# Kernel tuning notes

Hardware: AMD Instinct MI355X
Metric: run time of the kernel (lower is better)

## Reference

```python
import jax, jax.numpy as jnp
import numpy as np

TOTAL_MUONS = 2_000_000
BATCH = 16_384
FEAT = 3
COND = 4
NEG = -1.0e9


def _leaky(x):
    return jax.nn.leaky_relu(x, 0.2)


def setup_inputs() -> dict:
    key = jax.random.key(0)
    ks = jax.random.split(key, 12)
    flat_muons = jax.random.normal(ks[0], (TOTAL_MUONS, FEAT), dtype=jnp.float32)
    batch_index = jnp.sort(jax.random.randint(ks[1], (TOTAL_MUONS,), 0, BATCH)).astype(jnp.int64)
    conditions = jax.random.normal(ks[2], (BATCH, COND), dtype=jnp.float32)
    def lin(k, fan_in, fan_out):
        bound = 1.0 / np.sqrt(fan_in)
        kw, kb = jax.random.split(k)
        w = jax.random.uniform(kw, (fan_in, fan_out), jnp.float32, -bound, bound)
        b = jax.random.uniform(kb, (fan_out,), jnp.float32, -bound, bound)
        return w, b
    w1, b1 = lin(ks[3], FEAT + COND, 64)
    w2, b2 = lin(ks[4], 64, 128)
    w3, b3 = lin(ks[5], 128 + COND, 128)
    w4, b4 = lin(ks[6], 128, 1)
    return {"flat_muons": flat_muons, "batch_index": batch_index,
            "conditions": conditions, "batch_size": BATCH,
            "w1": w1, "b1": b1, "w2": w2, "b2": b2,
            "w3": w3, "b3": b3, "w4": w4, "b4": b4}


def reference(flat_muons, batch_index, conditions, batch_size,
              w1, b1, w2, b2, w3, b3, w4, b4):
    # gather event conditions per muon, concat with muon features
    flat_cond = conditions[batch_index]                       # [M, COND]
    point_input = jnp.concatenate([flat_muons, flat_cond], axis=1)
    # point network: Linear -> LeakyReLU(0.2) -> Linear -> LeakyReLU(0.2)
    h = _leaky(point_input @ w1 + b1)
    point_feats = _leaky(h @ w2 + b2)                         # [M, 128]
    point_feats = jnp.nan_to_num(point_feats, nan=0.0, posinf=0.0, neginf=0.0)
    # scatter-reduce amax with init -1e9 (include_self=True semantics)
    seg_max = jax.ops.segment_max(point_feats, batch_index, num_segments=batch_size)
    global_feats = jnp.maximum(seg_max, NEG)                  # [B, 128]
    global_feats = jnp.nan_to_num(global_feats, nan=NEG, posinf=-NEG, neginf=NEG)
    # decision network
    decision_input = jnp.concatenate([global_feats, conditions], axis=1)
    g = _leaky(decision_input @ w3 + b3)
    score = g @ w4 + b4                                       # [B, 1]
    score = score / max(1.0, float(batch_size) ** 0.5)
    return jnp.clip(score, -1000.0, 1000.0)
```

## Files before the change

kernel.cpp:

```cpp
#include <hip/hip_runtime.h>
#include <math.h>

#define NEGF (-1.0e9f)
#define NB 4

typedef __attribute__((ext_vector_type(8))) short short8;
typedef __attribute__((ext_vector_type(4))) float f32x4;

static __device__ __forceinline__ unsigned short bf16_rne(float f) {
    unsigned int u = __float_as_uint(f);
    u += 0x7FFFu + ((u >> 16) & 1u);
    return (unsigned short)(u >> 16);
}

__global__ void seg_bounds_kernel(const int* __restrict__ bi, int M, int B,
                                  int* __restrict__ seg) {
    int m = blockIdx.x * blockDim.x + threadIdx.x;
    if (m >= M) return;
    int cur = bi[m];
    if (m == 0) {
        for (int b = 0; b <= cur; ++b) seg[b] = 0;
    } else {
        int prev = bi[m - 1];
        for (int b = prev + 1; b <= cur; ++b) seg[b] = m;
    }
    if (m == M - 1) {
        for (int b = cur + 1; b <= B; ++b) seg[b] = M;
    }
}

__global__ void prep_w2_kernel(const float* __restrict__ w2,
                               unsigned short* __restrict__ wf) {
    int t = blockIdx.x * blockDim.x + threadIdx.x;
    if (t >= 8192) return;
    int e = t & 7, slot = (t >> 3) & 63, ks = (t >> 9) & 1, cg = t >> 10;
    int lane16 = slot & 15, kg = slot >> 4;
    int k = ks * 32 + kg * 8 + e;
    int col = cg * 16 + lane16;
    float w = w2[k * 128 + col];
    unsigned ub = __float_as_uint(w);
    unsigned short hi = (unsigned short)(ub >> 16);
    float lof = w - __uint_as_float(ub & 0xFFFF0000u);
    unsigned short lo = bf16_rne(lof);
    wf[((cg * 2 + ks) * 2 + 0) * 512 + slot * 8 + e] = hi;
    wf[((cg * 2 + ks) * 2 + 1) * 512 + slot * 8 + e] = lo;
}

__global__ __launch_bounds__(64, 2) void critic_kernel(
    const float* __restrict__ muons,
    const float* __restrict__ conds,
    const int*   __restrict__ seg,
    const float* __restrict__ w1,
    const float* __restrict__ b1,
    const unsigned short* __restrict__ w2frag,
    const float* __restrict__ b2,
    const float* __restrict__ w3,
    const float* __restrict__ b3,
    const float* __restrict__ w4,
    const float* __restrict__ b4,
    float* __restrict__ out,
    float scale, int Btot)
{
    __shared__ __align__(16) float w1t[64 * 8];
    __shared__ __align__(16) char  alds[2][4096];
    __shared__ float din[132];

    const int tid = threadIdx.x;
    const int l16 = tid & 15;
    const int lkg = tid >> 4;

    for (int idx = tid; idx < 512; idx += 64) {
        int k = idx >> 3, i = idx & 7;
        w1t[idx] = (i < 7) ? w1[i * 64 + k] : b1[k];
    }

    short8 bhi[8][2], blo[8][2];
    {
        const short8* wf = (const short8*)w2frag;
        #pragma unroll
        for (int cg = 0; cg < 8; ++cg) {
            #pragma unroll
            for (int ks = 0; ks < 2; ++ks) {
                bhi[cg][ks] = wf[((cg * 2 + ks) * 2 + 0) * 64 + tid];
                blo[cg][ks] = wf[((cg * 2 + ks) * 2 + 1) * 64 + tid];
            }
        }
    }
    __syncthreads();

    const int mslot = tid >> 1;
    const int half  = tid & 1;

    for (int bi = 0; bi < NB; ++bi) {
        const int b = blockIdx.x * NB + bi;
        if (b >= Btot) break;

        const float c0 = conds[b * 4 + 0];
        const float c1 = conds[b * 4 + 1];
        const float c2 = conds[b * 4 + 2];
        const float c3 = conds[b * 4 + 3];
        const int start = seg[b];
        const int end   = seg[b + 1];

        float gmax[8];
        #pragma unroll
        for (int cg = 0; cg < 8; ++cg) gmax[cg] = NEGF;

        for (int m0 = start; m0 < end; m0 += 32) {
            const int cnt = min(32, end - m0);

            if (mslot < cnt) {
                const int gm = m0 + mslot;
                const float x0 = muons[gm * 3 + 0];
                const float x1 = muons[gm * 3 + 1];
                const float x2 = muons[gm * 3 + 2];
                const unsigned swz = (unsigned)((mslot & 7) << 4);
                #pragma unroll
                for (int g = 0; g < 4; ++g) {
                    float hv[8];
                    #pragma unroll
                    for (int u = 0; u < 8; ++u) {
                        const float* wk = &w1t[(half * 32 + g * 8 + u) * 8];
                        float s = wk[7];
                        s = fmaf(x0, wk[0], s);
                        s = fmaf(x1, wk[1], s);
                        s = fmaf(x2, wk[2], s);
                        s = fmaf(c0, wk[3], s);
                        s = fmaf(c1, wk[4], s);
                        s = fmaf(c2, wk[5], s);
                        s = fmaf(c3, wk[6], s);
                        hv[u] = fmaxf(s, 0.2f * s);
                    }
                    short8 vhi, vlo;
                    #pragma unroll
                    for (int u = 0; u < 8; ++u) {
                        unsigned ub = __float_as_uint(hv[u]);
                        vhi[u] = (short)(ub >> 16);
                        float lof = hv[u] - __uint_as_float(ub & 0xFFFF0000u);
                        vlo[u] = (short)bf16_rne(lof);
                    }
                    const unsigned addr =
                        ((unsigned)(mslot * 128 + half * 64 + g * 16)) ^ swz;
                    *(short8*)(&alds[0][addr]) = vhi;
                    *(short8*)(&alds[1][addr]) = vlo;
                }
            }

            #pragma unroll
            for (int rt = 0; rt < 2; ++rt) {
                const int row = rt * 16 + l16;
                const unsigned base =
                    ((unsigned)(row * 128 + lkg * 16)) ^ ((unsigned)((row & 7) << 4));
                const short8 ah0 = *(const short8*)(&alds[0][base]);
                const short8 ah1 = *(const short8*)(&alds[0][base ^ 64u]);
                const short8 al0 = *(const short8*)(&alds[1][base]);
                const short8 al1 = *(const short8*)(&alds[1][base ^ 64u]);

                f32x4 acc[8];
                #pragma unroll
                for (int cg = 0; cg < 8; ++cg) {
                    f32x4 c = (f32x4){0.f, 0.f, 0.f, 0.f};
                    c = __builtin_amdgcn_mfma_f32_16x16x32_bf16(ah0, bhi[cg][0], c, 0, 0, 0);
                    c = __builtin_amdgcn_mfma_f32_16x16x32_bf16(ah1, bhi[cg][1], c, 0, 0, 0);
                    c = __builtin_amdgcn_mfma_f32_16x16x32_bf16(al0, bhi[cg][0], c, 0, 0, 0);
                    c = __builtin_amdgcn_mfma_f32_16x16x32_bf16(al1, bhi[cg][1], c, 0, 0, 0);
                    c = __builtin_amdgcn_mfma_f32_16x16x32_bf16(ah0, blo[cg][0], c, 0, 0, 0);
                    c = __builtin_amdgcn_mfma_f32_16x16x32_bf16(ah1, blo[cg][1], c, 0, 0, 0);
                    acc[cg] = c;
                }

                #pragma unroll
                for (int j = 0; j < 4; ++j) {
                    const int rowo = rt * 16 + lkg * 4 + j;
                    const bool act = rowo < cnt;
                    #pragma unroll
                    for (int cg = 0; cg < 8; ++cg)
                        gmax[cg] = fmaxf(gmax[cg], act ? acc[cg][j] : NEGF);
                }
            }
        }

        #pragma unroll
        for (int cg = 0; cg < 8; ++cg) {
            float v = gmax[cg];
            v = fmaxf(v, __shfl_xor(v, 16, 64));
            v = fmaxf(v, __shfl_xor(v, 32, 64));
            if (tid < 16) {
                const int col = cg * 16 + tid;
                const float biased = v + b2[col];
                const float actv = fmaxf(biased, 0.2f * biased);
                din[col] = (start < end) ? actv : NEGF;
            }
        }
        if (tid < 4) din[128 + tid] = conds[b * 4 + tid];

        float g0 = b3[tid];
        float g1 = b3[64 + tid];
        #pragma unroll 4
        for (int i = 0; i < 132; ++i) {
            const float d = din[i];
            g0 = fmaf(d, w3[i * 128 + tid], g0);
            g1 = fmaf(d, w3[i * 128 + 64 + tid], g1);
        }
        g0 = fmaxf(g0, 0.2f * g0);
        g1 = fmaxf(g1, 0.2f * g1);
        float part = g0 * w4[tid] + g1 * w4[64 + tid];
        #pragma unroll
        for (int s = 1; s < 64; s <<= 1)
            part += __shfl_xor(part, s, 64);
        if (tid == 0) {
            float sc = (part + b4[0]) * scale;
            out[b] = fminf(fmaxf(sc, -1000.0f), 1000.0f);
        }
    }
}

extern "C" void kernel_launch(void* const* d_in, const int* in_sizes, int n_in,
                              void* d_out, int out_size, void* d_ws, size_t ws_size,
                              hipStream_t stream) {
    const float* muons = (const float*)d_in[0];
    const int*   bidx  = (const int*)d_in[1];
    const float* conds = (const float*)d_in[2];
    const float* w1 = (const float*)d_in[4];
    const float* b1 = (const float*)d_in[5];
    const float* w2 = (const float*)d_in[6];
    const float* b2 = (const float*)d_in[7];
    const float* w3 = (const float*)d_in[8];
    const float* b3 = (const float*)d_in[9];
    const float* w4 = (const float*)d_in[10];
    const float* b4 = (const float*)d_in[11];

    const int M = in_sizes[0] / 3;
    const int B = in_sizes[2] / 4;
    int* seg = (int*)d_ws;
    const size_t off = (((size_t)(B + 1)) * 4 + 255) & ~(size_t)255;
    unsigned short* w2frag = (unsigned short*)((char*)d_ws + off);
    const float scale = 1.0f / fmaxf(1.0f, sqrtf((float)B));

    seg_bounds_kernel<<<(M + 255) / 256, 256, 0, stream>>>(bidx, M, B, seg);
    prep_w2_kernel<<<32, 256, 0, stream>>>(w2, w2frag);
    const int nblk = (B + NB - 1) / NB;
    critic_kernel<<<nblk, 64, 0, stream>>>(muons, conds, seg,
                                           w1, b1, w2frag, b2, w3, b3, w4, b4,
                                           (float*)d_out, scale, B);
}
```

Before: 280.2 us.

## Software-pipeline layer-1 compute of next muon tile behind MFMA layer-2

```diff
diff --git a/kernel.cpp b/kernel.cpp
--- a/kernel.cpp
+++ b/kernel.cpp
@@ -11,6 +11,12 @@
     unsigned int u = __float_as_uint(f);
     u += 0x7FFFu + ((u >> 16) & 1u);
     return (unsigned short)(u >> 16);
+}
+
+static __device__ __forceinline__ unsigned cvt_pk_bf16(float a, float b) {
+    unsigned r;
+    asm("v_cvt_pk_bf16_f32 %0, %1, %2" : "=v"(r) : "v"(a), "v"(b));
+    return r;
 }
 
 __global__ void seg_bounds_kernel(const int* __restrict__ bi, int M, int B,
@@ -68,6 +74,8 @@
     const int tid = threadIdx.x;
     const int l16 = tid & 15;
     const int lkg = tid >> 4;
+    const int mslot = tid >> 1;
+    const int half  = tid & 1;
 
     for (int idx = tid; idx < 512; idx += 64) {
         int k = idx >> 3, i = idx & 7;
@@ -88,8 +96,20 @@
     }
     __syncthreads();
 
-    const int mslot = tid >> 1;
-    const int half  = tid & 1;
+    unsigned wa[4];
+    {
+        const unsigned wsw = (unsigned)((mslot & 7) << 4);
+        #pragma unroll
+        for (int g = 0; g < 4; ++g)
+            wa[g] = ((unsigned)(mslot * 128 + half * 64 + g * 16)) ^ wsw;
+    }
+    unsigned rb[2];
+    #pragma unroll
+    for (int rt = 0; rt < 2; ++rt) {
+        const int row = rt * 16 + l16;
+        rb[rt] = ((unsigned)(row * 128 + lkg * 16)) ^ ((unsigned)((row & 7) << 4));
+    }
+    const float* w1h = w1t + half * 256;
 
     for (int bi = 0; bi < NB; ++bi) {
         const int b = blockIdx.x * NB + bi;
@@ -101,81 +121,128 @@
         const float c3 = conds[b * 4 + 3];
         const int start = seg[b];
         const int end   = seg[b + 1];
+        const int nrows = end - start;
+
+        auto l1_write = [&](float x0, float x1, float x2) {
+            #pragma unroll
+            for (int g = 0; g < 4; ++g) {
+                float hv[8];
+                #pragma unroll
+                for (int u = 0; u < 8; ++u) {
+                    const float* wk = &w1h[(g * 8 + u) * 8];
+                    float s = wk[7];
+                    s = fmaf(x0, wk[0], s);
+                    s = fmaf(x1, wk[1], s);
+                    s = fmaf(x2, wk[2], s);
+                    s = fmaf(c0, wk[3], s);
+                    s = fmaf(c1, wk[4], s);
+                    s = fmaf(c2, wk[5], s);
+                    s = fmaf(c3, wk[6], s);
+                    hv[u] = fmaxf(s, 0.2f * s);
+                }
+                unsigned hw0, hw1, hw2, hw3, lw0, lw1, lw2, lw3;
+                {
+                    unsigned h;
+                    h = cvt_pk_bf16(hv[0], hv[1]); hw0 = h;
+                    lw0 = cvt_pk_bf16(hv[0] - __uint_as_float(h << 16),
+                                      hv[1] - __uint_as_float(h & 0xFFFF0000u));
+                    h = cvt_pk_bf16(hv[2], hv[3]); hw1 = h;
+                    lw1 = cvt_pk_bf16(hv[2] - __uint_as_float(h << 16),
+                                      hv[3] - __uint_as_float(h & 0xFFFF0000u));
+                    h = cvt_pk_bf16(hv[4], hv[5]); hw2 = h;
+                    lw2 = cvt_pk_bf16(hv[4] - __uint_as_float(h << 16),
+                                      hv[5] - __uint_as_float(h & 0xFFFF0000u));
+                    h = cvt_pk_bf16(hv[6], hv[7]); hw3 = h;
+                    lw3 = cvt_pk_bf16(hv[6] - __uint_as_float(h << 16),
+                                      hv[7] - __uint_as_float(h & 0xFFFF0000u));
+                }
+                *(uint4*)(&alds[0][wa[g]]) = make_uint4(hw0, hw1, hw2, hw3);
+                *(uint4*)(&alds[1][wa[g]]) = make_uint4(lw0, lw1, lw2, lw3);
+            }
+        };
 
         float gmax[8];
         #pragma unroll
         for (int cg = 0; cg < 8; ++cg) gmax[cg] = NEGF;
 
-        for (int m0 = start; m0 < end; m0 += 32) {
-            const int cnt = min(32, end - m0);
-
-            if (mslot < cnt) {
-                const int gm = m0 + mslot;
-                const float x0 = muons[gm * 3 + 0];
-                const float x1 = muons[gm * 3 + 1];
-                const float x2 = muons[gm * 3 + 2];
-                const unsigned swz = (unsigned)((mslot & 7) << 4);
+        if (nrows > 0) {
+            const int ntiles = (nrows + 31) >> 5;
+
+            if (mslot < min(32, nrows)) {
+                const int gm = start + mslot;
+                l1_write(muons[gm * 3 + 0], muons[gm * 3 + 1], muons[gm * 3 + 2]);
+            }
+
+            for (int t = 0; t < ntiles; ++t) {
+                const int rem = nrows - t * 32;
+
+                short8 ah0[2], ah1[2], al0[2], al1[2];
                 #pragma unroll
-                for (int g = 0; g < 4; ++g) {
-                    float hv[8];
-                    #pragma unroll
-                    for (int u = 0; u < 8; ++u) {
-                        const float* wk = &w1t[(half * 32 + g * 8 + u) * 8];
-                        float s = wk[7];
-                        s = fmaf(x0, wk[0], s);
-                        s = fmaf(x1, wk[1], s);
-                        s = fmaf(x2, wk[2], s);
-                        s = fmaf(c0, wk[3], s);
-                        s = fmaf(c1, wk[4], s);
-                        s = fmaf(c2, wk[5], s);
-                        s = fmaf(c3, wk[6], s);
-                        hv[u] = fmaxf(s, 0.2f * s);
+                for (int rt = 0; rt < 2; ++rt) {
+                    ah0[rt] = *(const short8*)(&alds[0][rb[rt]]);
+                    ah1[rt] = *(const short8*)(&alds[0][rb[rt] ^ 64u]);
+                    al0[rt] = *(const short8*)(&alds[1][rb[rt]]);
+                    al1[rt] = *(const short8*)(&alds[1][rb[rt] ^ 64u]);
+                }
+
+                const bool hasN = rem > 32;
+                bool mv = false;
+                float xn0 = 0.f, xn1 = 0.f, xn2 = 0.f;
+                if (hasN) {
+                    mv = mslot < min(32, rem - 32);
+                    if (mv) {
+                        const int gm = start + t * 32 + 32 + mslot;
+                        xn0 = muons[gm * 3 + 0];
+                        xn1 = muons[gm * 3 + 1];
+                        xn2 = muons[gm * 3 + 2];
                     }
-                    short8 vhi, vlo;
-                    #pragma unroll
-                    for (int u = 0; u < 8; ++u) {
-                        unsigned ub = __float_as_uint(hv[u]);
-                        vhi[u] = (short)(ub >> 16);
-                        float lof = hv[u] - __uint_as_float(ub & 0xFFFF0000u);
-                        vlo[u] = (short)bf16_rne(lof);
-                    }
-                    const unsigned addr =
-                        ((unsigned)(mslot * 128 + half * 64 + g * 16)) ^ swz;
-                    *(short8*)(&alds[0][addr]) = vhi;
-                    *(short8*)(&alds[1][addr]) = vlo;
-                }
-            }
-
-            #pragma unroll
-            for (int rt = 0; rt < 2; ++rt) {
-                const int row = rt * 16 + l16;
-                const unsigned base =
-                    ((unsigned)(row * 128 + lkg * 16)) ^ ((unsigned)((row & 7) << 4));
-                const short8 ah0 = *(const short8*)(&alds[0][base]);
-                const short8 ah1 = *(const short8*)(&alds[0][base ^ 64u]);
-                const short8 al0 = *(const short8*)(&alds[1][base]);
-                const short8 al1 = *(const short8*)(&alds[1][base ^ 64u]);
-
-                f32x4 acc[8];
+                }
+
+                f32x4 acc0[8], acc1[8];
                 #pragma unroll
                 for (int cg = 0; cg < 8; ++cg) {
                     f32x4 c = (f32x4){0.f, 0.f, 0.f, 0.f};
-                    c = __builtin_amdgcn_mfma_f32_16x16x32_bf16(ah0, bhi[cg][0], c, 0, 0, 0);
-                    c = __builtin_amdgcn_mfma_f32_16x16x32_bf16(ah1, bhi[cg][1], c, 0, 0, 0);
-                    c = __builtin_amdgcn_mfma_f32_16x16x32_bf16(al0, bhi[cg][0], c, 0, 0, 0);
-                    c = __builtin_amdgcn_mfma_f32_16x16x32_bf16(al1, bhi[cg][1], c, 0, 0, 0);
-                    c = __builtin_amdgcn_mfma_f32_16x16x32_bf16(ah0, blo[cg][0], c, 0, 0, 0);
-                    c = __builtin_amdgcn_mfma_f32_16x16x32_bf16(ah1, blo[cg][1], c, 0, 0, 0);
-                    acc[cg] = c;
-                }
-
+                    c = __builtin_amdgcn_mfma_f32_16x16x32_bf16(ah0[0], bhi[cg][0], c, 0, 0, 0);
+                    c = __builtin_amdgcn_mfma_f32_16x16x32_bf16(ah1[0], bhi[cg][1], c, 0, 0, 0);
+                    c = __builtin_amdgcn_mfma_f32_16x16x32_bf16(al0[0], bhi[cg][0], c, 0, 0, 0);
+                    c = __builtin_amdgcn_mfma_f32_16x16x32_bf16(al1[0], bhi[cg][1], c, 0, 0, 0);
+                    c = __builtin_amdgcn_mfma_f32_16x16x32_bf16(ah0[0], blo[cg][0], c, 0, 0, 0);
+                    c = __builtin_amdgcn_mfma_f32_16x16x32_bf16(ah1[0], blo[cg][1], c, 0, 0, 0);
+                    acc0[cg] = c;
+                }
                 #pragma unroll
-                for (int j = 0; j < 4; ++j) {
-                    const int rowo = rt * 16 + lkg * 4 + j;
-                    const bool act = rowo < cnt;
+                for (int cg = 0; cg < 8; ++cg) {
+                    f32x4 c = (f32x4){0.f, 0.f, 0.f, 0.f};
+                    c = __builtin_amdgcn_mfma_f32_16x16x32_bf16(ah0[1], bhi[cg][0], c, 0, 0, 0);
+                    c = __builtin_amdgcn_mfma_f32_16x16x32_bf16(ah1[1], bhi[cg][1], c, 0, 0, 0);
+                    c = __builtin_amdgcn_mfma_f32_16x16x32_bf16(al0[1], bhi[cg][0], c, 0, 0, 0);
+                    c = __builtin_amdgcn_mfma_f32_16x16x32_bf16(al1[1], bhi[cg][1], c, 0, 0, 0);
+                    c = __builtin_amdgcn_mfma_f32_16x16x32_bf16(ah0[1], blo[cg][0], c, 0, 0, 0);
+                    c = __builtin_amdgcn_mfma_f32_16x16x32_bf16(ah1[1], blo[cg][1], c, 0, 0, 0);
+                    acc1[cg] = c;
+                }
+
+                if (mv) l1_write(xn0, xn1, xn2);
+
+                const int cnt = min(32, rem);
+                if (cnt == 32) {
                     #pragma unroll
                     for (int cg = 0; cg < 8; ++cg)
-                        gmax[cg] = fmaxf(gmax[cg], act ? acc[cg][j] : NEGF);
+                        #pragma unroll
+                        for (int j = 0; j < 4; ++j)
+                            gmax[cg] = fmaxf(gmax[cg],
+                                             fmaxf(acc0[cg][j], acc1[cg][j]));
+                } else {
+                    #pragma unroll
+                    for (int cg = 0; cg < 8; ++cg)
+                        #pragma unroll
+                        for (int j = 0; j < 4; ++j) {
+                            const int r0 = lkg * 4 + j;
+                            const int r1 = 16 + lkg * 4 + j;
+                            const float v0 = (r0 < cnt) ? acc0[cg][j] : NEGF;
+                            const float v1 = (r1 < cnt) ? acc1[cg][j] : NEGF;
+                            gmax[cg] = fmaxf(gmax[cg], fmaxf(v0, v1));
+                        }
                 }
             }
         }
@@ -189,7 +256,7 @@
                 const int col = cg * 16 + tid;
                 const float biased = v + b2[col];
                 const float actv = fmaxf(biased, 0.2f * biased);
-                din[col] = (start < end) ? actv : NEGF;
+                din[col] = (nrows > 0) ? actv : NEGF;
             }
         }
         if (tid < 4) din[128 + tid] = conds[b * 4 + tid];
```

Result: no change. 282.2 us (+0.7%).
